# Kernel optimization log

Measured on AMD Instinct MI355X. Metric: run time of the kernel, lower is better.

## Reference

```python
import jax, jax.numpy as jnp
import numpy as np

BSZ, SL, K, D_IN, D_OUT = 2, 1024, 24, 512, 512
K_U, K_Y = 3, 2
USE_HANKEL_L = False


def get_top_eigh(l, k, use_hankel_L):
    i = np.arange(1, l + 1, dtype=np.float64)
    s = i[:, None] + i[None, :]
    if use_hankel_L:
        Z = ((-1.0) ** (s - 2.0) + 1.0) * 8.0 / ((s + 3.0) * (s - 1.0) * (s + 1.0))
    else:
        Z = 2.0 / (s ** 3 - s)
    sigma, phi = np.linalg.eigh(Z)  # ascending
    return jnp.asarray(sigma[-k:], jnp.float32), jnp.asarray(phi[:, -k:], jnp.float32)


def shift(x, k):
    # causal shift along time axis 1, zero-padded at the front
    if k == 0:
        return x
    return jnp.pad(x, ((0, 0), (k, 0), (0, 0)))[:, : x.shape[1]]


def fft_causal_conv(filters, u):
    # filters: (l, k); u: (b, l, d) -> (b, l, k, d) causal convolution per filter
    l = u.shape[1]
    n = 2 * l
    F = jnp.fft.rfft(filters, n=n, axis=0)  # (n//2+1, k)
    U = jnp.fft.rfft(u, n=n, axis=1)        # (b, n//2+1, d)
    Y = jnp.fft.irfft(U[:, :, None, :] * F[None, :, :, None], n=n, axis=1)
    return Y[:, :l].astype(u.dtype)


def compute_ar_u(M_u, u):
    # ar_u[b,t,o] = sum_{i<k_u} M_u[i] @ u_{t-i}
    U = jnp.stack([shift(u, i) for i in range(M_u.shape[0])])  # (k_u, b, l, d_in)
    return jnp.einsum('koi,kbli->blo', M_u, U)


def compute_spectral(u, sigma, phi, M_phi_plus, M_phi_minus, m_y):
    l = u.shape[1]
    phi_s = phi * sigma ** 0.25  # eigenvalue-scaled spectral filters (l, k)
    U_plus = fft_causal_conv(phi_s, u)  # (b, l, k, d_in)
    spec = jnp.einsum('blki,koi->blo', U_plus, M_phi_plus)
    if not USE_HANKEL_L:
        # negative-featurization branch: filters modulated by (-1)^i
        alt = ((-1.0) ** jnp.arange(l)).astype(u.dtype)
        U_minus = fft_causal_conv(phi_s * alt[:, None], u)
        spec = spec + jnp.einsum('blki,koi->blo', U_minus, M_phi_minus)
    if m_y is not None:
        spec = shift(spec, m_y.shape[0])  # spectral features enter at lag k_y (paper: t-2)
    return spec


def compute_ar_y(m_y, y):
    # true short linear recurrence on outputs:
    # yhat_t = y_t + sum_{i=1}^{k_y} m_y[i-1] @ yhat_{t-i}; returns the correction term
    k_y, d_out = m_y.shape[0], m_y.shape[1]
    b = y.shape[0]

    def step(carry, y_t):  # carry: (k_y, b, d_out) = [yhat_{t-1}, ..., yhat_{t-k_y}]
        ar_t = jnp.einsum('koj,kbj->bo', m_y, carry)
        yhat_t = y_t + ar_t
        carry = jnp.concatenate([yhat_t[None], carry[:-1]], axis=0)
        return carry, ar_t

    y_tl = jnp.swapaxes(y, 0, 1)  # (l, b, d_out)
    _, ar = jax.lax.scan(step, jnp.zeros((k_y, b, d_out), y.dtype), y_tl)
    return jnp.swapaxes(ar, 0, 1)


def setup_inputs() -> dict:
    key = jax.random.key(0)
    k0, k1, k2, k3, k4 = jax.random.split(key, 5)
    inputs = jax.random.normal(k0, (BSZ, SL, D_IN), jnp.float32)
    M_u = jax.random.normal(k1, (K_U, D_OUT, D_IN), jnp.float32) * 0.02
    M_phi_plus = jax.random.normal(k2, (K, D_OUT, D_IN), jnp.float32) * 0.02
    M_phi_minus = jax.random.normal(k3, (K, D_OUT, D_IN), jnp.float32) * 0.02
    m_y = jax.random.normal(k4, (K_Y, D_OUT, D_OUT), jnp.float32) * 0.02
    sigma, phi = get_top_eigh(SL, K, USE_HANKEL_L)
    return {'inputs': inputs, 'M_u': M_u, 'M_phi_plus': M_phi_plus,
            'M_phi_minus': M_phi_minus, 'm_y': m_y, 'sigma': sigma, 'phi': phi}


def reference(inputs, M_u, M_phi_plus, M_phi_minus, m_y, sigma, phi):
    ar_u = compute_ar_u(M_u, inputs)
    spectral = compute_spectral(inputs, sigma, phi, M_phi_plus, M_phi_minus, m_y)
    y_t = ar_u + spectral
    y_t = y_t + compute_ar_y(m_y, y_t)  # learnable_m_y=True branch
    return y_t  # dropout p=0.0 (identity)
```

## Files before the change

kernel.cpp:

```cpp
#include <hip/hip_runtime.h>
#include <hip/hip_bf16.h>


typedef unsigned short u16;
typedef __attribute__((ext_vector_type(8))) short  vshort8;
typedef __attribute__((ext_vector_type(4))) short  vshort4;
typedef __attribute__((ext_vector_type(4))) float  f32x4;
typedef __attribute__((ext_vector_type(4))) unsigned int vuint4;

__device__ __forceinline__ u16 f2b(float x) {
  __hip_bfloat16 h = __float2bfloat16(x);
  return __builtin_bit_cast(u16, h);
}
__device__ __forceinline__ float b2f(u16 x) {
  unsigned int u = ((unsigned int)x) << 16;
  return __builtin_bit_cast(float, u);
}

__device__ __forceinline__ void gll16(const u16* g, u16* l) {
  __builtin_amdgcn_global_load_lds((__attribute__((address_space(1))) void*)g,
                                   (__attribute__((address_space(3))) void*)l,
                                   16, 0, 0);
}

struct GB {
  const u16* A; const u16* B;
  float* Cf; u16* Cb;
  const float* zf; float* out;
  u16* A2T; u16* Au;
  const u16* zp;
  int M, N;
};

template<int V>
__global__ __launch_bounds__(256) void g2(GB a) {
  const int tid = threadIdx.x;
  int bn = blockIdx.x, bm = blockIdx.y;
  const int bz = blockIdx.z;
  int cj = 0, cb = 0, cd = 0, slot = 0;
  int kbeg = 0, kend = 0;
  if (V == 0) { bm = blockIdx.x; bn = blockIdx.y; kend = 512; }
  if (V == 1) {
    int rest = blockIdx.x; bm = blockIdx.y;
    bn = rest & 3; cj = (rest >> 2) & 7;
    int chcb = rest >> 5;
    cd = bm - cj;
    if (cd < 0) return;
    cb = chcb & 1;
    slot = (chcb << 3) | cj;
    kbeg = (chcb >> 1) * 1536; kend = kbeg + 1536;
  }
  const int m0 = bm * 128, n0 = bn * 128;
  if (V == 2) {
    int jmax = (m0 >> 6) + 1;
    kbeg = bz * 2048;
    kend = kbeg + 2048;
    int tk = (jmax + 1) * 512;
    if (kend > tk) kend = tk;
    if (kend < kbeg) kend = kbeg;
  }
  if (V == 3 || V == 5 || V == 6 || V == 7) kend = 1024;

  __shared__ u16 lA[4096], lB[4096];
  f32x4 acc[4][4];
#pragma unroll
  for (int i = 0; i < 4; i++)
#pragma unroll
    for (int j = 0; j < 4; j++) acc[i][j] = f32x4{0.f, 0.f, 0.f, 0.f};

  const int lane = tid & 63, wv = tid >> 6, wr = wv >> 1, wc = wv & 1;
  const u16* Ap = a.A;
  if (V == 5) Ap = a.A + (size_t)bz * 524288;
  const u16* zp = a.zp + lane * 8;

  for (int k0 = kbeg; k0 < kend; k0 += 32) {
#pragma unroll
    for (int it = 0; it < 2; ++it) {
      const int weff = wv + it * 4;
      const int lrow = weff * 16 + (lane & 15);
      const int kk = k0 + ((lane >> 4) << 3);
      const u16* ga;
      if (V == 0) {
        ga = Ap + (size_t)(m0 + lrow) * 512 + kk;
      } else if (V == 1) {
        ga = Ap + (size_t)cd * 786432 + (size_t)lrow * 6144 + kk;
      } else if (V == 2) {
        int m = m0 + lrow, j = m >> 6, b = (m >> 5) & 1, c = m & 31;
        int tau = kk >> 9, p = kk & 511;
        ga = (tau > j) ? zp
                       : Ap + (size_t)(b * 1024 + c * 32 + j - tau) * 512 + p;
      } else if (V == 3) {
        int m = m0 + lrow;
        ga = (m < a.M) ? Ap + (size_t)m * 1024 + kk : zp;
      } else if (V == 5) {
        ga = Ap + (size_t)(m0 + lrow) * 1024 + kk;
      } else if (V == 6) {
        ga = (lrow < 64) ? Ap + (size_t)lrow * 1024 + kk : zp;
      } else {
        if (lrow < 32) {
          int b = lrow & 1, k2 = lrow >> 1;
          ga = Ap + (size_t)(b * 32 + 2 * k2) * 1024 + kk;
        } else ga = zp;
      }
      gll16(ga, &lA[weff * 512]);
      const int n = n0 + lrow;
      const u16* gb;
      if (V == 0) {
        gb = a.B + (size_t)n * 512 + kk;
      } else if (V == 1) {
        int kh = kk >> 7, sp = kk & 127;
        gb = a.B + (size_t)(cb * 512 + n) * 49152 + kh * 1024 + cj * 128 + sp;
      } else if (V == 2) {
        int tau = kk >> 9, p = kk & 511;
        gb = a.B + (size_t)tau * 524288 + (size_t)n * 1024 + p;
      } else if (V == 3) {
        int jn = n >> 9, o = n & 511;
        gb = a.B + (size_t)(jn + 1) * 524288 + (size_t)o * 1024 + kk;
      } else if (V == 5) {
        gb = a.B + (size_t)n * 1024 + kk;
      } else {
        gb = (n < 512)
            ? a.B + (size_t)32 * 524288 + (size_t)n * 1024 + kk
            : a.B + (size_t)31 * 524288 + (size_t)(n - 512) * 1024 + kk;
      }
      gll16(gb, &lB[weff * 512]);
    }
    __syncthreads();
    vshort8 af[4], bf_[4];
#pragma unroll
    for (int s = 0; s < 4; s++) {
      af[s]  = *(const vshort8*)&lA[(((wr * 4 + s) * 4 + (lane >> 4)) * 16 + (lane & 15)) * 8];
      bf_[s] = *(const vshort8*)&lB[(((wc * 4 + s) * 4 + (lane >> 4)) * 16 + (lane & 15)) * 8];
    }
#pragma unroll
    for (int i = 0; i < 4; i++)
#pragma unroll
      for (int j = 0; j < 4; j++)
        acc[i][j] = __builtin_amdgcn_mfma_f32_16x16x32_bf16(af[i], bf_[j], acc[i][j], 0, 0, 0);
    __syncthreads();
  }

#pragma unroll
  for (int i = 0; i < 4; i++) {
    int em = m0 + wr * 64 + i * 16 + ((lane >> 4) << 2);
#pragma unroll
    for (int j = 0; j < 4; j++) {
      int n = n0 + wc * 64 + j * 16 + (lane & 15);
      f32x4 v = acc[i][j];
      if (V == 0) {
        int b = em >> 10, s = em & 1023;
        if (n < 24576) {
          int kh = n >> 9, o = n & 511;
          vshort4 pk = { (short)f2b(v[0]), (short)f2b(v[1]), (short)f2b(v[2]), (short)f2b(v[3]) };
          *(vshort4*)(&a.A2T[(size_t)(b * 512 + o) * 49152 + (size_t)kh * 1024 + s]) = pk;
        } else {
          int jj = (n - 24576) >> 9, o = n & 511;
#pragma unroll
          for (int t = 0; t < 4; t++)
            a.Au[((size_t)(b * 3 + jj) * 1024 + (s + t)) * 512 + o] = f2b(v[t]);
        }
      } else if (V == 1) {
        u16* C = a.Cb + (size_t)slot * 524288;
#pragma unroll
        for (int t = 0; t < 4; t++) C[(size_t)(em + t) * 512 + n] = f2b(v[t]);
      } else if (V == 2) {
        float* C = a.Cf + (size_t)bz * 1048576;
#pragma unroll
        for (int t = 0; t < 4; t++) C[(size_t)(em + t) * 512 + n] = v[t];
      } else if (V == 3) {
        int jj = n >> 9, oo = n & 511;
#pragma unroll
        for (int t = 0; t < 4; t++) {
          int m = em + t;
          if (m < a.M) {
            int b = m >> 5, c = m & 31;
            float zv = a.zf[(size_t)(jj * 64 + b * 32 + c) * 512 + oo];
            a.out[(size_t)b * 524288 + (size_t)(c * 32 + jj) * 512 + oo] = v[t] + zv;
          }
        }
      } else if (V == 5) {
        u16* C = a.Cb + (size_t)bz * 524288;
#pragma unroll
        for (int t = 0; t < 4; t++) C[(size_t)(em + t) * 1024 + n] = f2b(v[t]);
      } else if (V == 6) {
        int jrow = (n < 512) ? 31 : 30, oo = n & 511;
#pragma unroll
        for (int t = 0; t < 4; t++) {
          int m = em + t;
          if (m < 62) {
            int b = m & 1, c = m >> 1;
            a.Cf[(size_t)m * 1024 + n] =
                v[t] + a.zf[(size_t)(jrow * 64 + b * 32 + (c + 1)) * 512 + oo];
          }
        }
      } else {
        int jrow = (n < 512) ? 31 : 30, oo = n & 511;
#pragma unroll
        for (int t = 0; t < 4; t++) {
          int m = em + t;
          if (m < 32) {
            int b = m & 1, k2 = m >> 1;
            float val = v[t] + a.zf[(size_t)(jrow * 64 + b * 32 + 2 * k2) * 512 + oo];
            a.Cb[(size_t)(b * 32 + 2 * k2 + 1) * 1024 + n] = f2b(val);
          }
        }
      }
    }
  }
}

__global__ void k_prep_X(const float* __restrict__ u, u16* __restrict__ X, int n) {
  int i = blockIdx.x * 256 + threadIdx.x;
  if (i < n) X[i] = f2b(u[i]);
}

__global__ void k_prep_phis(const float* __restrict__ phi, const float* __restrict__ sigma,
                            float* __restrict__ phis) {
  int i = blockIdx.x * 256 + threadIdx.x;
  if (i >= 1024 * 48) return;
  int tau = i / 48, kf = i % 48, k = (kf >= 24) ? kf - 24 : kf;
  float v = phi[tau * 24 + k] * powf(sigma[k], 0.25f);
  if (kf >= 24 && (tau & 1)) v = -v;
  phis[i] = v;
}

__global__ void k_prep_W1(const float* __restrict__ Mp, const float* __restrict__ Mm,
                          const float* __restrict__ Mu, u16* __restrict__ W1) {
  int i = blockIdx.x * 256 + threadIdx.x;
  if (i >= 13369344) return;
  float v;
  if (i < 6291456) v = Mp[i];
  else if (i < 12582912) v = Mm[i - 6291456];
  else v = Mu[i - 12582912];
  W1[i] = f2b(v);
}

__global__ void k_prep_Wtoep(const float* __restrict__ phis, u16* __restrict__ W) {
  int i = blockIdx.x * 256 + threadIdx.x;
  if (i >= 6291456) return;
  int kap = i % 6144, row = i / 6144;
  int tp = row & 127, d = row >> 7;
  int kh = kap >> 7, sp = kap & 127;
  int tau = d * 128 + tp - sp;
  W[i] = (tau >= 0 && tau < 1024) ? f2b(phis[tau * 48 + kh]) : (u16)0;
}

__global__ void k_initTop(const float* __restrict__ my, u16* __restrict__ Top) {
  int i = blockIdx.x * 256 + threadIdx.x;
  if (i >= 1048576) return;
  int mat = i >> 19, rem = i & 524287, o = rem >> 10, k = rem & 1023;
  u16 v;
  if (mat == 0) v = (k == o) ? (u16)0x3F80 : (u16)0;
  else v = (k < 512) ? f2b(my[o * 512 + k]) : f2b(my[262144 + o * 512 + (k - 512)]);
  Top[i] = v;
}

__global__ __launch_bounds__(256) void k_transT(const u16* __restrict__ Top,
                                                u16* __restrict__ STc, int c) {
  __shared__ u16 tile[64][72];
  int tx = blockIdx.x, ty = blockIdx.y;
  int tid = threadIdx.x;
  int r = tid >> 2, seg = tid & 3;
  int k = ty * 64 + r;
  const u16* src = (k < 512) ? Top + (size_t)c * 524288 + (size_t)k * 1024 + tx * 64
                             : Top + (size_t)(c - 1) * 524288 + (size_t)(k - 512) * 1024 + tx * 64;
  *(vuint4*)&tile[r][seg * 16]     = *(const vuint4*)(src + seg * 16);
  *(vuint4*)&tile[r][seg * 16 + 8] = *(const vuint4*)(src + seg * 16 + 8);
  __syncthreads();
  int n = tx * 64 + r;
  u16 tmp[16];
#pragma unroll
  for (int j = 0; j < 16; j++) tmp[j] = tile[seg * 16 + j][r];
  *(vuint4*)&STc[(size_t)n * 1024 + ty * 64 + seg * 16]     = *(vuint4*)&tmp[0];
  *(vuint4*)&STc[(size_t)n * 1024 + ty * 64 + seg * 16 + 8] = *(vuint4*)&tmp[8];
}

__device__ __forceinline__ void addp(float* acc, vuint4 v) {
  const unsigned int* vu = (const unsigned int*)&v;
#pragma unroll
  for (int e = 0; e < 4; ++e) {
    unsigned int pw = vu[e];
    acc[2 * e]     += __builtin_bit_cast(float, (pw & 0xffffu) << 16);
    acc[2 * e + 1] += __builtin_bit_cast(float, pw & 0xffff0000u);
  }
}

__global__ void k_combine(const u16* __restrict__ parts, const u16* __restrict__ Au,
                          u16* __restrict__ ybf) {
  int i = blockIdx.x * 256 + threadIdx.x;
  if (i >= 131072) return;
  int og = i & 63, t = (i >> 6) & 1023, b = i >> 16;
  float acc[8];
#pragma unroll
  for (int e = 0; e < 8; ++e) acc[e] = 0.f;
#pragma unroll
  for (int j = 0; j < 3; j++)
    if (t >= j)
      addp(acc, *(const vuint4*)(Au + ((size_t)(b * 3 + j) * 1024 + (t - j)) * 512 + og * 8));
  if (t >= 2) {
    int tp = t - 2, bmv = tp >> 7;
    for (int g = 0; g < 8; ++g) {
      const u16* base = parts + (size_t)(b * 0 + g * 8) * 524288 + (size_t)tp * 512 + og * 8;
      if ((g & 1) != b) continue;
      for (int j = 0; j <= bmv; ++j)
        addp(acc, *(const vuint4*)(base + (size_t)j * 524288));
    }
  }
  u16 o16[8];
#pragma unroll
  for (int e = 0; e < 8; ++e) o16[e] = f2b(acc[e]);
  *(vuint4*)(ybf + ((size_t)(b * 1024 + t)) * 512 + og * 8) = *(vuint4*)o16;
}

__global__ void k_zreduce(const float* __restrict__ zp, float* __restrict__ z) {
  int i = blockIdx.x * 256 + threadIdx.x;
  if (i >= 1048576) return;
  float s = 0.f;
#pragma unroll
  for (int j = 0; j < 8; j++) s += zp[(size_t)j * 1048576 + i];
  z[i] = s;
}

__global__ void k_wm(const float* __restrict__ zf, u16* __restrict__ Wm) {
  int i = blockIdx.x * 256 + threadIdx.x;
  if (i >= 65536) return;
  int row = i >> 10, n = i & 1023;
  int b = row & 1, c = row >> 1;
  int jrow = (n < 512) ? 31 : 30, oo = n & 511;
  Wm[i] = f2b(zf[(size_t)(jrow * 64 + b * 32 + c) * 512 + oo]);
}

__global__ __launch_bounds__(256) void k_bnd2(const u16* __restrict__ Top,
                                              const float* __restrict__ ubuf,
                                              float* __restrict__ bnd,
                                              u16* __restrict__ Abnd, int k) {
  __shared__ float st[2048];
  int tid = threadIdx.x;
  const float* s0 = bnd + (size_t)k * 2048;
  for (int j = tid; j < 2048; j += 256) st[j] = s0[j];
  __syncthreads();
  int q4 = blockIdx.x * 256 + tid;
  int q = q4 >> 2, quarter = q4 & 3;
  int b = q >> 10, kk = q & 1023;
  const u16* row = (kk < 512) ? Top + (size_t)64 * 524288 + (size_t)kk * 1024
                              : Top + (size_t)63 * 524288 + (size_t)(kk - 512) * 1024;
  const float* stb = st + b * 1024 + quarter * 256;
  const u16* rp = row + quarter * 256;
  float sum = 0.f;
  for (int t = 0; t < 32; ++t) {
    vuint4 v = *(const vuint4*)(rp + t * 8);
    const unsigned int* vu = (const unsigned int*)&v;
#pragma unroll
    for (int e = 0; e < 4; ++e) {
      unsigned int pw = vu[e];
      float lo = __builtin_bit_cast(float, (pw & 0xffffu) << 16);
      float hi = __builtin_bit_cast(float, pw & 0xffff0000u);
      sum += lo * stb[t * 8 + e * 2] + hi * stb[t * 8 + e * 2 + 1];
    }
  }
  sum += __shfl_xor(sum, 1);
  sum += __shfl_xor(sum, 2);
  if (quarter == 0) {
    float s = sum + ubuf[(size_t)(4 * k + b) * 1024 + kk];
    bnd[(size_t)(k + 1) * 2048 + b * 1024 + kk] = s;
    Abnd[(size_t)(b * 32 + 2 * k + 2) * 1024 + kk] = f2b(s);
  }
}

extern "C" void kernel_launch(void* const* d_in, const int* in_sizes, int n_in,
                              void* d_out, int out_size, void* d_ws, size_t ws_size,
                              hipStream_t stream) {
  const float* u     = (const float*)d_in[0];
  const float* Mu    = (const float*)d_in[1];
  const float* Mp    = (const float*)d_in[2];
  const float* Mm    = (const float*)d_in[3];
  const float* my    = (const float*)d_in[4];
  const float* sigma = (const float*)d_in[5];
  const float* phi   = (const float*)d_in[6];
  float* out = (float*)d_out;

  char* ws = (char*)d_ws;
  size_t off = 0;
  auto alc = [&](size_t b) { size_t p = off; off = (off + b + 255) & ~(size_t)255; return p; };
  u16*  X     = (u16*)(ws + alc(2097152));
  u16*  Wtoep = (u16*)(ws + alc(12582912));
  u16*  A2T   = (u16*)(ws + alc(100663296));
  u16*  Au    = (u16*)(ws + alc(6291456));
  u16*  W1    = (u16*)(ws + alc(26738688));
  char* ptail = ws + alc(40370176); (void)ptail;
  float* phis = (float*)(ws + alc(196608));
  float* bnd  = (float*)(ws + alc(131072));
  u16*  Abnd  = (u16*)(ws + alc(131072));
  u16*  Wm    = (u16*)(ws + alc(131072));
  float* ubuf = (float*)(ws + alc(262144));
  u16*  zpad  = (u16*)(ws + alc(32768));
  if (off > ws_size) return;
  u16*  partsBf = (u16*)W1;
  float* zparts = (float*)W1;
  u16*  ybf = A2T;
  float* zf = (float*)((char*)A2T + (4 << 20));
  u16*  Top = (u16*)((char*)A2T + (size_t)(8 << 20));
  u16*  STc = (u16*)((char*)A2T + (size_t)(76 << 20));

  hipMemsetAsync(zpad, 0, 32768, stream);

  k_prep_X<<<dim3(4096), 256, 0, stream>>>(u, X, 1048576);
  k_prep_phis<<<dim3(192), 256, 0, stream>>>(phi, sigma, phis);
  k_prep_W1<<<dim3(52224), 256, 0, stream>>>(Mp, Mm, Mu, W1);
  k_prep_Wtoep<<<dim3(24576), 256, 0, stream>>>(phis, Wtoep);

  {
    GB g{}; g.A = X; g.B = W1; g.A2T = A2T; g.Au = Au; g.zp = zpad;
    g.M = 2048; g.N = 26112;
    g2<0><<<dim3(16, 204, 1), 256, 0, stream>>>(g);
  }
  {
    GB g{}; g.A = Wtoep; g.B = A2T; g.Cb = partsBf; g.zp = zpad;
    g.M = 1024; g.N = 512;
    g2<1><<<dim3(256, 8, 1), 256, 0, stream>>>(g);
  }
  k_combine<<<dim3(512), 256, 0, stream>>>(partsBf, Au, ybf);

  k_initTop<<<dim3(4096), 256, 0, stream>>>(my, Top);
  {
    const int cs[5] = {1, 2, 4, 8, 16};
    for (int li = 0; li < 5; ++li) {
      int c = cs[li];
      k_transT<<<dim3(16, 16), 256, 0, stream>>>(Top, STc, c);
      GB s{}; s.A = Top + 524288; s.B = STc; s.Cb = Top + (size_t)(c + 1) * 524288;
      s.zp = zpad; s.M = 512; s.N = 1024;
      g2<5><<<dim3(8, 4, c), 256, 0, stream>>>(s);
    }
    k_transT<<<dim3(16, 16), 256, 0, stream>>>(Top, STc, 32);
    GB s{}; s.A = Top + (size_t)31 * 524288; s.B = STc;
    s.Cb = Top + (size_t)63 * 524288; s.zp = zpad; s.M = 512; s.N = 1024;
    g2<5><<<dim3(8, 4, 2), 256, 0, stream>>>(s);
  }

  {
    GB g{}; g.A = ybf; g.B = Top; g.Cf = zparts; g.zp = zpad; g.M = 2048; g.N = 512;
    g2<2><<<dim3(4, 16, 8), 256, 0, stream>>>(g);
  }
  k_zreduce<<<dim3(4096), 256, 0, stream>>>(zparts, zf);

  k_wm<<<dim3(256), 256, 0, stream>>>(zf, Wm);
  {
    GB g{}; g.A = Wm; g.B = Top; g.Cf = ubuf; g.zf = zf; g.zp = zpad;
    g.M = 64; g.N = 1024;
    g2<6><<<dim3(8, 1, 1), 256, 0, stream>>>(g);
  }
  hipMemsetAsync(bnd, 0, 8192, stream);
  hipMemsetAsync(Abnd, 0, 131072, stream);
  for (int k = 0; k < 15; ++k)
    k_bnd2<<<dim3(32), 256, 0, stream>>>(Top, ubuf, bnd, Abnd, k);
  {
    GB g{}; g.A = Abnd; g.B = Top; g.Cb = Abnd; g.zf = zf; g.zp = zpad;
    g.M = 32; g.N = 1024;
    g2<7><<<dim3(8, 1, 1), 256, 0, stream>>>(g);
  }

  {
    GB g{}; g.A = Abnd; g.B = Top; g.zf = zf; g.out = out; g.zp = zpad;
    g.M = 64; g.N = 16384;
    g2<3><<<dim3(128, 1, 1), 256, 0, stream>>>(g);
  }
}
```

Before: 858.8 us.

## Double-buffer GEMM tiles via registers and compact triangular Toeplitz grid

Replaces direct global-to-LDS loads with register-staged loads into a double-buffered LDS tile, so the next K-slice is fetched while MFMAs run on the current one. The V1 Toeplitz GEMM now launches only the lower-triangular blocks, indexed by a sqrt-based mapping, and uses 3072-long K chunks across four z slices. That removes early-exit blocks and halves the partial-sum count that k_combine reads. In exchange it doubles LDS use, adds register pressure, and replaces the zero-pad buffer with conditional zero fills.

```diff
diff --git a/kernel.cpp b/kernel.cpp
--- a/kernel.cpp
+++ b/kernel.cpp
@@ -17,18 +17,11 @@
   return __builtin_bit_cast(float, u);
 }
 
-__device__ __forceinline__ void gll16(const u16* g, u16* l) {
-  __builtin_amdgcn_global_load_lds((__attribute__((address_space(1))) void*)g,
-                                   (__attribute__((address_space(3))) void*)l,
-                                   16, 0, 0);
-}
-
 struct GB {
   const u16* A; const u16* B;
   float* Cf; u16* Cb;
   const float* zf; float* out;
   u16* A2T; u16* Au;
-  const u16* zp;
   int M, N;
 };
 
@@ -41,14 +34,13 @@
   int kbeg = 0, kend = 0;
   if (V == 0) { bm = blockIdx.x; bn = blockIdx.y; kend = 512; }
   if (V == 1) {
-    int rest = blockIdx.x; bm = blockIdx.y;
-    bn = rest & 3; cj = (rest >> 2) & 7;
-    int chcb = rest >> 5;
-    cd = bm - cj;
-    if (cd < 0) return;
-    cb = chcb & 1;
-    slot = (chcb << 3) | cj;
-    kbeg = (chcb >> 1) * 1536; kend = kbeg + 1536;
+    int p = blockIdx.x;
+    bm = (int)((sqrtf(8.f * (float)p + 1.f) - 1.f) * 0.5f);
+    cj = p - (bm * (bm + 1)) / 2;
+    bn = blockIdx.y;
+    cb = bz & 1; cd = bm - cj;
+    slot = bz * 8 + cj;
+    kbeg = (bz >> 1) * 3072; kend = kbeg + 3072;
   }
   const int m0 = bm * 128, n0 = bn * 128;
   if (V == 2) {
@@ -61,7 +53,7 @@
   }
   if (V == 3 || V == 5 || V == 6 || V == 7) kend = 1024;
 
-  __shared__ u16 lA[4096], lB[4096];
+  __shared__ u16 lA[2][4096], lB[2][4096];
   f32x4 acc[4][4];
 #pragma unroll
   for (int i = 0; i < 4; i++)
@@ -71,73 +63,89 @@
   const int lane = tid & 63, wv = tid >> 6, wr = wv >> 1, wc = wv & 1;
   const u16* Ap = a.A;
   if (V == 5) Ap = a.A + (size_t)bz * 524288;
-  const u16* zp = a.zp + lane * 8;
-
+
+  auto gaddrA = [&](int it, int k0) -> const u16* {
+    int lrow = (it * 4 + wv) * 16 + (lane & 15);
+    int kk = k0 + ((lane >> 4) << 3);
+    if (V == 0) return Ap + (size_t)(m0 + lrow) * 512 + kk;
+    if (V == 1) return Ap + (size_t)cd * 786432 + (size_t)lrow * 6144 + kk;
+    if (V == 2) {
+      int m = m0 + lrow, j = m >> 6, b = (m >> 5) & 1, c = m & 31;
+      int tau = kk >> 9, p = kk & 511;
+      if (tau > j) return nullptr;
+      return Ap + (size_t)(b * 1024 + c * 32 + j - tau) * 512 + p;
+    }
+    if (V == 3) { int m = m0 + lrow; return (m < a.M) ? Ap + (size_t)m * 1024 + kk : nullptr; }
+    if (V == 5) return Ap + (size_t)(m0 + lrow) * 1024 + kk;
+    if (V == 6) return (lrow < 64) ? Ap + (size_t)lrow * 1024 + kk : nullptr;
+    if (lrow < 32) {
+      int b = lrow & 1, k2 = lrow >> 1;
+      return Ap + (size_t)(b * 32 + 2 * k2) * 1024 + kk;
+    }
+    return nullptr;
+  };
+  auto gaddrB = [&](int it, int k0) -> const u16* {
+    int lrow = (it * 4 + wv) * 16 + (lane & 15);
+    int kk = k0 + ((lane >> 4) << 3);
+    int n = n0 + lrow;
+    if (V == 0) return a.B + (size_t)n * 512 + kk;
+    if (V == 1) {
+      int kh = kk >> 7, sp = kk & 127;
+      return a.B + (size_t)(cb * 512 + n) * 49152 + kh * 1024 + cj * 128 + sp;
+    }
+    if (V == 2) {
+      int tau = kk >> 9, p = kk & 511;
+      return a.B + (size_t)tau * 524288 + (size_t)n * 1024 + p;
+    }
+    if (V == 3) {
+      int jn = n >> 9, o = n & 511;
+      return a.B + (size_t)(jn + 1) * 524288 + (size_t)o * 1024 + kk;
+    }
+    if (V == 5) return a.B + (size_t)n * 1024 + kk;
+    return (n < 512)
+        ? a.B + (size_t)32 * 524288 + (size_t)n * 1024 + kk
+        : a.B + (size_t)31 * 524288 + (size_t)(n - 512) * 1024 + kk;
+  };
+
+  vuint4 ra[2] = {vuint4{0,0,0,0}, vuint4{0,0,0,0}};
+  vuint4 rb[2] = {vuint4{0,0,0,0}, vuint4{0,0,0,0}};
+  auto loadtile = [&](int k0) {
+#pragma unroll
+    for (int it = 0; it < 2; ++it) {
+      const u16* pa = gaddrA(it, k0);
+      ra[it] = pa ? *(const vuint4*)pa : vuint4{0u, 0u, 0u, 0u};
+      rb[it] = *(const vuint4*)gaddrB(it, k0);
+    }
+  };
+  auto writetile = [&](int c) {
+#pragma unroll
+    for (int it = 0; it < 2; ++it) {
+      *(vuint4*)&lA[c][it * 2048 + tid * 8] = ra[it];
+      *(vuint4*)&lB[c][it * 2048 + tid * 8] = rb[it];
+    }
+  };
+
+  if (kbeg < kend) loadtile(kbeg);
+  writetile(0);
+  __syncthreads();
+  int cur = 0;
   for (int k0 = kbeg; k0 < kend; k0 += 32) {
-#pragma unroll
-    for (int it = 0; it < 2; ++it) {
-      const int weff = wv + it * 4;
-      const int lrow = weff * 16 + (lane & 15);
-      const int kk = k0 + ((lane >> 4) << 3);
-      const u16* ga;
-      if (V == 0) {
-        ga = Ap + (size_t)(m0 + lrow) * 512 + kk;
-      } else if (V == 1) {
-        ga = Ap + (size_t)cd * 786432 + (size_t)lrow * 6144 + kk;
-      } else if (V == 2) {
-        int m = m0 + lrow, j = m >> 6, b = (m >> 5) & 1, c = m & 31;
-        int tau = kk >> 9, p = kk & 511;
-        ga = (tau > j) ? zp
-                       : Ap + (size_t)(b * 1024 + c * 32 + j - tau) * 512 + p;
-      } else if (V == 3) {
-        int m = m0 + lrow;
-        ga = (m < a.M) ? Ap + (size_t)m * 1024 + kk : zp;
-      } else if (V == 5) {
-        ga = Ap + (size_t)(m0 + lrow) * 1024 + kk;
-      } else if (V == 6) {
-        ga = (lrow < 64) ? Ap + (size_t)lrow * 1024 + kk : zp;
-      } else {
-        if (lrow < 32) {
-          int b = lrow & 1, k2 = lrow >> 1;
-          ga = Ap + (size_t)(b * 32 + 2 * k2) * 1024 + kk;
-        } else ga = zp;
-      }
-      gll16(ga, &lA[weff * 512]);
-      const int n = n0 + lrow;
-      const u16* gb;
-      if (V == 0) {
-        gb = a.B + (size_t)n * 512 + kk;
-      } else if (V == 1) {
-        int kh = kk >> 7, sp = kk & 127;
-        gb = a.B + (size_t)(cb * 512 + n) * 49152 + kh * 1024 + cj * 128 + sp;
-      } else if (V == 2) {
-        int tau = kk >> 9, p = kk & 511;
-        gb = a.B + (size_t)tau * 524288 + (size_t)n * 1024 + p;
-      } else if (V == 3) {
-        int jn = n >> 9, o = n & 511;
-        gb = a.B + (size_t)(jn + 1) * 524288 + (size_t)o * 1024 + kk;
-      } else if (V == 5) {
-        gb = a.B + (size_t)n * 1024 + kk;
-      } else {
-        gb = (n < 512)
-            ? a.B + (size_t)32 * 524288 + (size_t)n * 1024 + kk
-            : a.B + (size_t)31 * 524288 + (size_t)(n - 512) * 1024 + kk;
-      }
-      gll16(gb, &lB[weff * 512]);
-    }
-    __syncthreads();
+    bool hasnext = (k0 + 32 < kend);
+    if (hasnext) loadtile(k0 + 32);
     vshort8 af[4], bf_[4];
 #pragma unroll
     for (int s = 0; s < 4; s++) {
-      af[s]  = *(const vshort8*)&lA[(((wr * 4 + s) * 4 + (lane >> 4)) * 16 + (lane & 15)) * 8];
-      bf_[s] = *(const vshort8*)&lB[(((wc * 4 + s) * 4 + (lane >> 4)) * 16 + (lane & 15)) * 8];
+      af[s]  = *(const vshort8*)&lA[cur][(((wr * 4 + s) * 4 + (lane >> 4)) * 16 + (lane & 15)) * 8];
+      bf_[s] = *(const vshort8*)&lB[cur][(((wc * 4 + s) * 4 + (lane >> 4)) * 16 + (lane & 15)) * 8];
     }
 #pragma unroll
     for (int i = 0; i < 4; i++)
 #pragma unroll
       for (int j = 0; j < 4; j++)
         acc[i][j] = __builtin_amdgcn_mfma_f32_16x16x32_bf16(af[i], bf_[j], acc[i][j], 0, 0, 0);
+    if (hasnext) writetile(cur ^ 1);
     __syncthreads();
+    cur ^= 1;
   }
 
 #pragma unroll
@@ -299,9 +307,10 @@
       addp(acc, *(const vuint4*)(Au + ((size_t)(b * 3 + j) * 1024 + (t - j)) * 512 + og * 8));
   if (t >= 2) {
     int tp = t - 2, bmv = tp >> 7;
-    for (int g = 0; g < 8; ++g) {
-      const u16* base = parts + (size_t)(b * 0 + g * 8) * 524288 + (size_t)tp * 512 + og * 8;
+#pragma unroll
+    for (int g = 0; g < 4; ++g) {
       if ((g & 1) != b) continue;
+      const u16* base = parts + (size_t)(g * 8) * 524288 + (size_t)tp * 512 + og * 8;
       for (int j = 0; j <= bmv; ++j)
         addp(acc, *(const vuint4*)(base + (size_t)j * 524288));
     }
@@ -393,7 +402,6 @@
   u16*  Abnd  = (u16*)(ws + alc(131072));
   u16*  Wm    = (u16*)(ws + alc(131072));
   float* ubuf = (float*)(ws + alc(262144));
-  u16*  zpad  = (u16*)(ws + alc(32768));
   if (off > ws_size) return;
   u16*  partsBf = (u16*)W1;
   float* zparts = (float*)W1;
@@ -402,22 +410,20 @@
   u16*  Top = (u16*)((char*)A2T + (size_t)(8 << 20));
   u16*  STc = (u16*)((char*)A2T + (size_t)(76 << 20));
 
-  hipMemsetAsync(zpad, 0, 32768, stream);
-
   k_prep_X<<<dim3(4096), 256, 0, stream>>>(u, X, 1048576);
   k_prep_phis<<<dim3(192), 256, 0, stream>>>(phi, sigma, phis);
   k_prep_W1<<<dim3(52224), 256, 0, stream>>>(Mp, Mm, Mu, W1);
   k_prep_Wtoep<<<dim3(24576), 256, 0, stream>>>(phis, Wtoep);
 
   {
-    GB g{}; g.A = X; g.B = W1; g.A2T = A2T; g.Au = Au; g.zp = zpad;
+    GB g{}; g.A = X; g.B = W1; g.A2T = A2T; g.Au = Au;
     g.M = 2048; g.N = 26112;
     g2<0><<<dim3(16, 204, 1), 256, 0, stream>>>(g);
   }
   {
-    GB g{}; g.A = Wtoep; g.B = A2T; g.Cb = partsBf; g.zp = zpad;
+    GB g{}; g.A = Wtoep; g.B = A2T; g.Cb = partsBf;
     g.M = 1024; g.N = 512;
-    g2<1><<<dim3(256, 8, 1), 256, 0, stream>>>(g);
+    g2<1><<<dim3(36, 4, 4), 256, 0, stream>>>(g);
   }
   k_combine<<<dim3(512), 256, 0, stream>>>(partsBf, Au, ybf);
 
@@ -428,24 +434,24 @@
       int c = cs[li];
       k_transT<<<dim3(16, 16), 256, 0, stream>>>(Top, STc, c);
       GB s{}; s.A = Top + 524288; s.B = STc; s.Cb = Top + (size_t)(c + 1) * 524288;
-      s.zp = zpad; s.M = 512; s.N = 1024;
+      s.M = 512; s.N = 1024;
       g2<5><<<dim3(8, 4, c), 256, 0, stream>>>(s);
     }
     k_transT<<<dim3(16, 16), 256, 0, stream>>>(Top, STc, 32);
     GB s{}; s.A = Top + (size_t)31 * 524288; s.B = STc;
-    s.Cb = Top + (size_t)63 * 524288; s.zp = zpad; s.M = 512; s.N = 1024;
+    s.Cb = Top + (size_t)63 * 524288; s.M = 512; s.N = 1024;
     g2<5><<<dim3(8, 4, 2), 256, 0, stream>>>(s);
   }
 
   {
-    GB g{}; g.A = ybf; g.B = Top; g.Cf = zparts; g.zp = zpad; g.M = 2048; g.N = 512;
+    GB g{}; g.A = ybf; g.B = Top; g.Cf = zparts; g.M = 2048; g.N = 512;
     g2<2><<<dim3(4, 16, 8), 256, 0, stream>>>(g);
   }
   k_zreduce<<<dim3(4096), 256, 0, stream>>>(zparts, zf);
 
   k_wm<<<dim3(256), 256, 0, stream>>>(zf, Wm);
   {
-    GB g{}; g.A = Wm; g.B = Top; g.Cf = ubuf; g.zf = zf; g.zp = zpad;
+    GB g{}; g.A = Wm; g.B = Top; g.Cf = ubuf; g.zf = zf;
     g.M = 64; g.N = 1024;
     g2<6><<<dim3(8, 1, 1), 256, 0, stream>>>(g);
   }
@@ -454,13 +460,13 @@
   for (int k = 0; k < 15; ++k)
     k_bnd2<<<dim3(32), 256, 0, stream>>>(Top, ubuf, bnd, Abnd, k);
   {
-    GB g{}; g.A = Abnd; g.B = Top; g.Cb = Abnd; g.zf = zf; g.zp = zpad;
+    GB g{}; g.A = Abnd; g.B = Top; g.Cb = Abnd; g.zf = zf;
     g.M = 32; g.N = 1024;
     g2<7><<<dim3(8, 1, 1), 256, 0, stream>>>(g);
   }
 
   {
-    GB g{}; g.A = Abnd; g.B = Top; g.zf = zf; g.out = out; g.zp = zpad;
+    GB g{}; g.A = Abnd; g.B = Top; g.zf = zf; g.out = out;
     g.M = 64; g.N = 16384;
     g2<3><<<dim3(128, 1, 1), 256, 0, stream>>>(g);
   }
```

New measurement: 769.1 us. 10.4% less time.
